# Kernel tuning notes

Hardware: AMD Instinct MI355X
Metric: run time of the kernel (lower is better)

Reference implementation:

```python
import jax, jax.numpy as jnp
import numpy as np

HIGHEST = jax.lax.Precision.HIGHEST
KEY_CHUNK_SIZE = 4096 * 4  # hard-coded in the module's __call__
HEADS = 8
DIM_HEAD = 64


def _query_chunk_size(num_q: int) -> int:
    # replicates the module's static chunk-size selection
    if num_q % 64 == 0:
        return num_q // 64
    if num_q % 16 == 0:
        return num_q // 16
    if num_q % 4 == 0:
        return num_q // 4
    return num_q


def _me_attention(q, k, v, q_chunk: int, k_chunk: int):
    # q, k, v: (S, H, D) where H here is the flattened batch*heads axis
    S, H, D = q.shape
    num_kv = k.shape[0]
    k_chunk = min(k_chunk, num_kv)
    q = q / jnp.sqrt(jnp.asarray(D, q.dtype))
    kc = k.reshape(-1, k_chunk, H, D)          # (nk, kc, H, D)
    vc = v.reshape(-1, k_chunk, H, v.shape[-1])

    def per_qchunk(qch):  # qch: (qc, H, D)
        def summarize(args):
            kch, vch = args
            s = jnp.einsum('qhd,khd->qhk', qch, kch, precision=HIGHEST)
            m = jax.lax.stop_gradient(jnp.max(s, axis=-1, keepdims=True))
            e = jnp.exp(s - m)
            ev = jnp.einsum('khf,qhk->qhf', vch, e, precision=HIGHEST)
            return ev, e.sum(axis=-1), m[..., 0]
        evs, ews, ms = jax.lax.map(summarize, (kc, vc))  # stacked over key chunks
        gm = jnp.max(ms, axis=0)                # (qc, H) global running max
        sc = jnp.exp(ms - gm)                   # (nk, qc, H) rescale factors
        num = (evs * sc[..., None]).sum(axis=0)
        den = (ews * sc).sum(axis=0)
        return num / den[..., None]

    qs = q.reshape(-1, q_chunk, H, D)
    out = jax.lax.map(per_qchunk, qs)           # (nq, qc, H, F)
    return out.reshape(S, H, -1)


def _forward(hidden_states, w_q, w_k, w_v, w_out, b_out):
    B, S, Dm = hidden_states.shape
    H, dh = HEADS, DIM_HEAD
    q = hidden_states @ w_q
    k = hidden_states @ w_k
    v = hidden_states @ w_v

    def to_heads(t):  # (B,S,H*dh) -> (B*H, S, dh)
        return t.reshape(B, S, H, dh).transpose(0, 2, 1, 3).reshape(B * H, S, dh)

    qs, ks, vs = to_heads(q), to_heads(k), to_heads(v)
    # module transposes to (S, B*H, dh) before memory-efficient attention
    qcs = _query_chunk_size(S)
    attn = _me_attention(qs.transpose(1, 0, 2), ks.transpose(1, 0, 2),
                         vs.transpose(1, 0, 2), qcs, KEY_CHUNK_SIZE)
    attn = attn.transpose(1, 0, 2)  # (B*H, S, dh)
    attn = attn.reshape(B, H, S, dh).transpose(0, 2, 1, 3).reshape(B, S, H * dh)
    return attn @ w_out + b_out


def setup_inputs() -> dict:
    key = jax.random.key(0)
    ks = jax.random.split(key, 6)
    B, S, Dm = 2, 8192, 512
    inner = HEADS * DIM_HEAD  # 512
    return {
        'hidden_states': jax.random.normal(ks[0], (B, S, Dm), dtype=jnp.float32),
        'w_q': jax.random.normal(ks[1], (Dm, inner), dtype=jnp.float32) * 0.02,
        'w_k': jax.random.normal(ks[2], (Dm, inner), dtype=jnp.float32) * 0.02,
        'w_v': jax.random.normal(ks[3], (Dm, inner), dtype=jnp.float32) * 0.02,
        'w_out': jax.random.normal(ks[4], (inner, Dm), dtype=jnp.float32) * 0.02,
        'b_out': jnp.zeros((Dm,), dtype=jnp.float32),
    }


def reference(hidden_states, w_q, w_k, w_v, w_out, b_out):
    return _forward(hidden_states, w_q, w_k, w_v, w_out, b_out)
```

## Files before the change

kernel.cpp:

```cpp
#include <hip/hip_runtime.h>
#include <stdint.h>

typedef unsigned short u16;
typedef __attribute__((ext_vector_type(8))) short short8;
typedef __attribute__((ext_vector_type(4))) short short4v;
typedef __attribute__((ext_vector_type(4))) float f32x4;

#define MFMA16(a, b, c) __builtin_amdgcn_mfma_f32_16x16x16bf16_1k(a, b, c, 0, 0, 0)
#define MFMA32(a, b, c) __builtin_amdgcn_mfma_f32_16x16x32_bf16(a, b, c, 0, 0, 0)

#if __has_builtin(__builtin_amdgcn_exp2f)
#define EXP2F(x) __builtin_amdgcn_exp2f(x)
#else
#define EXP2F(x) exp2f(x)
#endif

#define ASYNC16(G, L)                                                            \
    __builtin_amdgcn_global_load_lds((const __attribute__((address_space(1))) void*)(const void*)(G), \
                                     (__attribute__((address_space(3))) void*)(void*)(L), 16, 0, 0)

__device__ __forceinline__ u16 f2bf(float f) {
    union { float f; uint32_t u; } c; c.f = f;
    uint32_t r = (c.u + 0x7fffu + ((c.u >> 16) & 1u)) >> 16;
    return (u16)r;
}

__global__ __launch_bounds__(256) void k_convert_x(const float* __restrict__ X, u16* __restrict__ Xb) {
    int idx = blockIdx.x * 256 + threadIdx.x;
    float4 v = ((const float4*)X)[idx];
    union { u16 s[4]; uint2 v; } u;
    u.s[0] = f2bf(v.x); u.s[1] = f2bf(v.y); u.s[2] = f2bf(v.z); u.s[3] = f2bf(v.w);
    ((uint2*)Xb)[idx] = u.v;
}

__global__ __launch_bounds__(256) void k_convert_w(const float* __restrict__ W0, const float* __restrict__ W1,
                                                   const float* __restrict__ W2, const float* __restrict__ W3,
                                                   u16* __restrict__ Wt) {
    __shared__ u16 T[64][72];
    const float* W = (blockIdx.z == 0) ? W0 : (blockIdx.z == 1) ? W1 : (blockIdx.z == 2) ? W2 : W3;
    int k0 = blockIdx.x * 64, n0 = blockIdx.y * 64;
    int t = threadIdx.x;
    for (int i = 0; i < 4; i++) {
        int id = t + i * 256;
        int row = id >> 4, c4 = (id & 15) * 4;
        float4 v = *(const float4*)(W + (size_t)(k0 + row) * 512 + n0 + c4);
        union { u16 s[4]; uint2 v; } u;
        u.s[0] = f2bf(v.x); u.s[1] = f2bf(v.y); u.s[2] = f2bf(v.z); u.s[3] = f2bf(v.w);
        *(uint2*)&T[row][c4] = u.v;
    }
    __syncthreads();
    u16* O = Wt + (size_t)blockIdx.z * 512 * 512;
    for (int i = 0; i < 2; i++) {
        int id = t + i * 256;
        int row = id >> 3, c8 = (id & 7) * 8;
        union { u16 s[8]; uint4 v; } tmp;
        for (int j = 0; j < 8; j++) tmp.s[j] = T[c8 + j][row];
        *(uint4*)(O + (size_t)(n0 + row) * 512 + k0 + c8) = tmp.v;
    }
}

__global__ __launch_bounds__(256) void k_gemm_qkv(const u16* __restrict__ X, const u16* __restrict__ Wt,
                                                  u16* __restrict__ Q, u16* __restrict__ K, u16* __restrict__ V) {
    __shared__ u16 As[128][40];
    __shared__ u16 Bs[128][40];
    const int t = threadIdx.x;
    const int wave = t >> 6, lane = t & 63, quad = lane >> 4, l16 = lane & 15;
    const int wm = (wave >> 1) * 64, wn = (wave & 1) * 64;
    const int m0 = blockIdx.x * 128, n0 = blockIdx.y * 128;
    const u16* Bt = Wt + (size_t)blockIdx.z * 262144;
    const f32x4 fz = {0.f, 0.f, 0.f, 0.f};
    f32x4 acc[4][4];
    for (int i = 0; i < 4; i++) for (int j = 0; j < 4; j++) acc[i][j] = fz;
    for (int k0 = 0; k0 < 512; k0 += 32) {
        __syncthreads();
        for (int i = 0; i < 2; i++) {
            int id = t + i * 256;
            int row = id >> 2, c8 = (id & 3) * 8;
            *(uint4*)&As[row][c8] = *(const uint4*)(X + (size_t)(m0 + row) * 512 + k0 + c8);
            *(uint4*)&Bs[row][c8] = *(const uint4*)(Bt + (size_t)(n0 + row) * 512 + k0 + c8);
        }
        __syncthreads();
        short8 af[4], bf[4];
        for (int mt = 0; mt < 4; mt++) af[mt] = *(const short8*)&As[wm + mt * 16 + l16][quad * 8];
        for (int nt = 0; nt < 4; nt++) bf[nt] = *(const short8*)&Bs[wn + nt * 16 + l16][quad * 8];
        for (int mt = 0; mt < 4; mt++)
            for (int nt = 0; nt < 4; nt++)
                acc[mt][nt] = MFMA32(af[mt], bf[nt], acc[mt][nt]);
    }
    const float scale = (blockIdx.z == 0) ? 0.18033688011112042f : 1.0f;
    u16* Out = (blockIdx.z == 0) ? Q : (blockIdx.z == 1) ? K : V;
    for (int mt = 0; mt < 4; mt++)
        for (int nt = 0; nt < 4; nt++)
            for (int r = 0; r < 4; r++) {
                int m = m0 + wm + mt * 16 + quad * 4 + r;
                int n = n0 + wn + nt * 16 + l16;
                int b = m >> 13, s = m & 8191, h = n >> 6, d = n & 63;
                Out[((size_t)((b * 8 + h) * 8192 + s)) * 64 + d] = f2bf(acc[mt][nt][r] * scale);
            }
}

__global__ __launch_bounds__(256) void k_transpose_v(const u16* __restrict__ V, u16* __restrict__ Vt) {
    __shared__ u16 T[64][72];
    int s0 = blockIdx.x * 64, bh = blockIdx.y;
    int t = threadIdx.x;
    for (int i = 0; i < 2; i++) {
        int id = t + i * 256, row = id >> 3, c8 = (id & 7) * 8;
        *(uint4*)&T[row][c8] = *(const uint4*)(V + ((size_t)bh * 8192 + s0 + row) * 64 + c8);
    }
    __syncthreads();
    for (int i = 0; i < 2; i++) {
        int id = t + i * 256, row = id >> 3, c8 = (id & 7) * 8;
        union { u16 s[8]; uint4 v; } tmp;
        for (int j = 0; j < 8; j++) tmp.s[j] = T[c8 + j][row];
        *(uint4*)(Vt + ((size_t)bh * 64 + row) * 8192 + s0 + c8) = tmp.v;
    }
}

__global__ __launch_bounds__(256, 4) void k_flash(const u16* __restrict__ Q, const u16* __restrict__ K,
                                                  const u16* __restrict__ Vt, u16* __restrict__ Attn) {
    __shared__ u16 KsAll[2][4096];
    __shared__ u16 VsAll[2][4096];
    const int t = threadIdx.x;
    const int wave = t >> 6, lane = t & 63, quad = lane >> 4, l16 = lane & 15;
    const int l7 = l16 & 7, q1 = quad >> 1, q0 = quad & 1;
    const int qblk = blockIdx.x, bh = blockIdx.y;
    const int b = bh >> 3, h = bh & 7;
    const int q0g = qblk * 128;
    const int mq = wave * 32;
    const u16* Qb = Q + ((size_t)bh * 8192 + q0g) * 64;
    const u16* Kb = K + (size_t)bh * 8192 * 64;
    const u16* Vb = Vt + (size_t)bh * 64 * 8192;

    const int r0 = t >> 3, r1 = (t + 256) >> 3;
    const int x0 = ((t & 7) ^ (r0 & 7)) * 8;
    const int x1 = ((t & 7) ^ (r1 & 7)) * 8;
    const u16* gK0 = Kb + r0 * 64 + x0;
    const u16* gK1 = Kb + r1 * 64 + x1;
    const u16* gV0 = Vb + (size_t)r0 * 8192 + x0;
    const u16* gV1 = Vb + (size_t)r1 * 8192 + x1;
    u16* lK = &KsAll[0][0] + t * 8;
    u16* lV = &VsAll[0][0] + t * 8;

    auto prefetch = [&](int it, int buf) {
        ASYNC16(gK0 + it * 4096, lK + buf * 4096);
        ASYNC16(gK1 + it * 4096, lK + buf * 4096 + 2048);
        ASYNC16(gV0 + it * 64,   lV + buf * 4096);
        ASYNC16(gV1 + it * 64,   lV + buf * 4096 + 2048);
    };

    short8 qf[2][2];
    for (int mt = 0; mt < 2; mt++)
        for (int ks = 0; ks < 2; ks++)
            qf[mt][ks] = *(const short8*)(Qb + (size_t)(mq + mt * 16 + l16) * 64 + ks * 32 + quad * 8);

    const short4v ones = {0x3F80, 0x3F80, 0x3F80, 0x3F80};
    const f32x4 fz = {0.f, 0.f, 0.f, 0.f};
    f32x4 o[2][4], l_i[2];
    for (int mt = 0; mt < 2; mt++) l_i[mt] = fz;
    for (int mt = 0; mt < 2; mt++) for (int nt = 0; nt < 4; nt++) o[mt][nt] = fz;

    prefetch(0, 0);

    auto body = [&](int it, int buf) {
        __syncthreads();
        if (it != 127) prefetch(it + 1, buf ^ 1);
        const u16* KsB = &KsAll[buf][0];
        const u16* VsB = &VsAll[buf][0];

        f32x4 sc[2][4];
        for (int mt = 0; mt < 2; mt++) for (int kt = 0; kt < 4; kt++) sc[mt][kt] = fz;
        for (int ks = 0; ks < 2; ks++)
            for (int kt = 0; kt < 4; kt++) {
                short8 kf = *(const short8*)(KsB + kt * 1024 + l16 * 64 + (((ks * 4 + quad) ^ l7) * 8));
                sc[0][kt] = MFMA32(kf, qf[0][ks], sc[0][kt]);
                sc[1][kt] = MFMA32(kf, qf[1][ks], sc[1][kt]);
            }

        short4v pf[2][4];
        for (int mt = 0; mt < 2; mt++)
            for (int kt = 0; kt < 4; kt++) {
                union { float f; uint32_t u; } e0, e1, e2, e3;
                e0.f = EXP2F(sc[mt][kt][0]);
                e1.f = EXP2F(sc[mt][kt][1]);
                e2.f = EXP2F(sc[mt][kt][2]);
                e3.f = EXP2F(sc[mt][kt][3]);
                union { uint32_t u[2]; short4v s; } pk;
                pk.u[0] = __builtin_amdgcn_perm(e1.u, e0.u, 0x07060302);
                pk.u[1] = __builtin_amdgcn_perm(e3.u, e2.u, 0x07060302);
                pf[mt][kt] = pk.s;
            }

        for (int mt = 0; mt < 2; mt++) {
            f32x4 lacc = fz;
            for (int kt = 0; kt < 4; kt++) lacc = MFMA16(pf[mt][kt], ones, lacc);
            for (int r = 0; r < 4; r++) l_i[mt][r] += lacc[r];
        }

        for (int kt = 0; kt < 4; kt++)
            for (int nt = 0; nt < 4; nt++) {
                short4v vf = *(const short4v*)(VsB + nt * 1024 + l16 * 64 + (((kt * 2 + q1) ^ l7) * 8) + q0 * 4);
                o[0][nt] = MFMA16(pf[0][kt], vf, o[0][nt]);
                o[1][nt] = MFMA16(pf[1][kt], vf, o[1][nt]);
            }
    };

    for (int it2 = 0; it2 < 64; it2++) {
        body(2 * it2, 0);
        body(2 * it2 + 1, 1);
    }

    for (int mt = 0; mt < 2; mt++) {
        f32x4 inv;
        for (int r = 0; r < 4; r++) inv[r] = 1.0f / l_i[mt][r];
        for (int nt = 0; nt < 4; nt++)
            for (int r = 0; r < 4; r++) {
                int sg = q0g + mq + mt * 16 + quad * 4 + r;
                int n = h * 64 + nt * 16 + l16;
                Attn[((size_t)(b * 8192 + sg)) * 512 + n] = f2bf(o[mt][nt][r] * inv[r]);
            }
    }
}

__global__ __launch_bounds__(256) void k_gemm_out(const u16* __restrict__ A, const u16* __restrict__ Wot,
                                                  const float* __restrict__ bias, float* __restrict__ Out) {
    __shared__ u16 As[128][40];
    __shared__ u16 Bs[128][40];
    const int t = threadIdx.x;
    const int wave = t >> 6, lane = t & 63, quad = lane >> 4, l16 = lane & 15;
    const int wm = (wave >> 1) * 64, wn = (wave & 1) * 64;
    const int m0 = blockIdx.x * 128, n0 = blockIdx.y * 128;
    const f32x4 fz = {0.f, 0.f, 0.f, 0.f};
    f32x4 acc[4][4];
    for (int i = 0; i < 4; i++) for (int j = 0; j < 4; j++) acc[i][j] = fz;
    for (int k0 = 0; k0 < 512; k0 += 32) {
        __syncthreads();
        for (int i = 0; i < 2; i++) {
            int id = t + i * 256;
            int row = id >> 2, c8 = (id & 3) * 8;
            *(uint4*)&As[row][c8] = *(const uint4*)(A + (size_t)(m0 + row) * 512 + k0 + c8);
            *(uint4*)&Bs[row][c8] = *(const uint4*)(Wot + (size_t)(n0 + row) * 512 + k0 + c8);
        }
        __syncthreads();
        short8 af[4], bf[4];
        for (int mt = 0; mt < 4; mt++) af[mt] = *(const short8*)&As[wm + mt * 16 + l16][quad * 8];
        for (int nt = 0; nt < 4; nt++) bf[nt] = *(const short8*)&Bs[wn + nt * 16 + l16][quad * 8];
        for (int mt = 0; mt < 4; mt++)
            for (int nt = 0; nt < 4; nt++)
                acc[mt][nt] = MFMA32(af[mt], bf[nt], acc[mt][nt]);
    }
    float bv[4];
    for (int nt = 0; nt < 4; nt++) bv[nt] = bias[n0 + wn + nt * 16 + l16];
    for (int mt = 0; mt < 4; mt++)
        for (int nt = 0; nt < 4; nt++)
            for (int r = 0; r < 4; r++) {
                int m = m0 + wm + mt * 16 + quad * 4 + r;
                int n = n0 + wn + nt * 16 + l16;
                Out[(size_t)m * 512 + n] = acc[mt][nt][r] + bv[nt];
            }
}

extern "C" void kernel_launch(void* const* d_in, const int* in_sizes, int n_in,
                              void* d_out, int out_size, void* d_ws, size_t ws_size,
                              hipStream_t stream) {
    const float* X   = (const float*)d_in[0];
    const float* w_q = (const float*)d_in[1];
    const float* w_k = (const float*)d_in[2];
    const float* w_v = (const float*)d_in[3];
    const float* w_o = (const float*)d_in[4];
    const float* b_o = (const float*)d_in[5];
    float* Out = (float*)d_out;

    char* ws = (char*)d_ws;
    u16* Xb   = (u16*)(ws);
    u16* Wt   = (u16*)(ws + 16777216);
    u16* Qd   = (u16*)(ws + 18874368);
    u16* Kd   = (u16*)(ws + 35651584);
    u16* Vd   = (u16*)(ws + 52428800);
    u16* Vtd  = (u16*)(ws + 69206016);
    u16* Attn = Xb;

    hipLaunchKernelGGL(k_convert_x, dim3(8192), dim3(256), 0, stream, X, Xb);
    hipLaunchKernelGGL(k_convert_w, dim3(8, 8, 4), dim3(256), 0, stream, w_q, w_k, w_v, w_o, Wt);
    hipLaunchKernelGGL(k_gemm_qkv, dim3(128, 4, 3), dim3(256), 0, stream, Xb, Wt, Qd, Kd, Vd);
    hipLaunchKernelGGL(k_transpose_v, dim3(128, 16), dim3(256), 0, stream, Vd, Vtd);
    hipLaunchKernelGGL(k_flash, dim3(64, 16), dim3(256), 0, stream, Qd, Kd, Vtd, Attn);
    hipLaunchKernelGGL(k_gemm_out, dim3(128, 4), dim3(256), 0, stream, Attn, Wt + 3 * 262144, b_o, Out);
}
```

Baseline: 464.2 us.

## Widen flash block to 8 waves sharing K/V tiles; compute row sums on VALU

The attention kernel now launches 512-thread blocks covering 256 queries instead of 256-thread blocks covering 128. Eight waves share each staged K/V tile, which halves global-to-LDS traffic per query, and each thread issues one async load per tensor per step instead of two. The softmax denominator is no longer computed with extra MFMAs against a ones vector. Each lane accumulates scalar exp sums instead, and the per-query totals are combined with cross-lane shuffles in the epilogue. In exchange, larger blocks with launch bounds (512,4) may raise register pressure or lower scheduling flexibility, and the VALU adds take the place of the matrix-core work.

```diff
diff --git a/kernel.cpp b/kernel.cpp
--- a/kernel.cpp
+++ b/kernel.cpp
@@ -116,36 +116,31 @@
     }
 }
 
-__global__ __launch_bounds__(256, 4) void k_flash(const u16* __restrict__ Q, const u16* __restrict__ K,
+__global__ __launch_bounds__(512, 4) void k_flash(const u16* __restrict__ Q, const u16* __restrict__ K,
                                                   const u16* __restrict__ Vt, u16* __restrict__ Attn) {
     __shared__ u16 KsAll[2][4096];
     __shared__ u16 VsAll[2][4096];
     const int t = threadIdx.x;
     const int wave = t >> 6, lane = t & 63, quad = lane >> 4, l16 = lane & 15;
-    const int l7 = l16 & 7, q1 = quad >> 1, q0 = quad & 1;
+    const int l7 = l16 & 7, q1 = quad >> 1, qlo = quad & 1;
     const int qblk = blockIdx.x, bh = blockIdx.y;
     const int b = bh >> 3, h = bh & 7;
-    const int q0g = qblk * 128;
+    const int q0g = qblk * 256;
     const int mq = wave * 32;
     const u16* Qb = Q + ((size_t)bh * 8192 + q0g) * 64;
     const u16* Kb = K + (size_t)bh * 8192 * 64;
     const u16* Vb = Vt + (size_t)bh * 64 * 8192;
 
-    const int r0 = t >> 3, r1 = (t + 256) >> 3;
+    const int r0 = t >> 3;
     const int x0 = ((t & 7) ^ (r0 & 7)) * 8;
-    const int x1 = ((t & 7) ^ (r1 & 7)) * 8;
     const u16* gK0 = Kb + r0 * 64 + x0;
-    const u16* gK1 = Kb + r1 * 64 + x1;
     const u16* gV0 = Vb + (size_t)r0 * 8192 + x0;
-    const u16* gV1 = Vb + (size_t)r1 * 8192 + x1;
     u16* lK = &KsAll[0][0] + t * 8;
     u16* lV = &VsAll[0][0] + t * 8;
 
     auto prefetch = [&](int it, int buf) {
         ASYNC16(gK0 + it * 4096, lK + buf * 4096);
-        ASYNC16(gK1 + it * 4096, lK + buf * 4096 + 2048);
         ASYNC16(gV0 + it * 64,   lV + buf * 4096);
-        ASYNC16(gV1 + it * 64,   lV + buf * 4096 + 2048);
     };
 
     short8 qf[2][2];
@@ -153,10 +148,9 @@
         for (int ks = 0; ks < 2; ks++)
             qf[mt][ks] = *(const short8*)(Qb + (size_t)(mq + mt * 16 + l16) * 64 + ks * 32 + quad * 8);
 
-    const short4v ones = {0x3F80, 0x3F80, 0x3F80, 0x3F80};
     const f32x4 fz = {0.f, 0.f, 0.f, 0.f};
-    f32x4 o[2][4], l_i[2];
-    for (int mt = 0; mt < 2; mt++) l_i[mt] = fz;
+    f32x4 o[2][4];
+    float l_i[2] = {0.f, 0.f};
     for (int mt = 0; mt < 2; mt++) for (int nt = 0; nt < 4; nt++) o[mt][nt] = fz;
 
     prefetch(0, 0);
@@ -168,13 +162,14 @@
         const u16* VsB = &VsAll[buf][0];
 
         f32x4 sc[2][4];
-        for (int mt = 0; mt < 2; mt++) for (int kt = 0; kt < 4; kt++) sc[mt][kt] = fz;
-        for (int ks = 0; ks < 2; ks++)
-            for (int kt = 0; kt < 4; kt++) {
-                short8 kf = *(const short8*)(KsB + kt * 1024 + l16 * 64 + (((ks * 4 + quad) ^ l7) * 8));
-                sc[0][kt] = MFMA32(kf, qf[0][ks], sc[0][kt]);
-                sc[1][kt] = MFMA32(kf, qf[1][ks], sc[1][kt]);
-            }
+        for (int kt = 0; kt < 4; kt++) {
+            short8 kf0 = *(const short8*)(KsB + kt * 1024 + l16 * 64 + (((0 * 4 + quad) ^ l7) * 8));
+            short8 kf1 = *(const short8*)(KsB + kt * 1024 + l16 * 64 + (((1 * 4 + quad) ^ l7) * 8));
+            sc[0][kt] = MFMA32(kf0, qf[0][0], fz);
+            sc[1][kt] = MFMA32(kf0, qf[1][0], fz);
+            sc[0][kt] = MFMA32(kf1, qf[0][1], sc[0][kt]);
+            sc[1][kt] = MFMA32(kf1, qf[1][1], sc[1][kt]);
+        }
 
         short4v pf[2][4];
         for (int mt = 0; mt < 2; mt++)
@@ -184,21 +179,16 @@
                 e1.f = EXP2F(sc[mt][kt][1]);
                 e2.f = EXP2F(sc[mt][kt][2]);
                 e3.f = EXP2F(sc[mt][kt][3]);
+                l_i[mt] += (e0.f + e1.f) + (e2.f + e3.f);
                 union { uint32_t u[2]; short4v s; } pk;
                 pk.u[0] = __builtin_amdgcn_perm(e1.u, e0.u, 0x07060302);
                 pk.u[1] = __builtin_amdgcn_perm(e3.u, e2.u, 0x07060302);
                 pf[mt][kt] = pk.s;
             }
 
-        for (int mt = 0; mt < 2; mt++) {
-            f32x4 lacc = fz;
-            for (int kt = 0; kt < 4; kt++) lacc = MFMA16(pf[mt][kt], ones, lacc);
-            for (int r = 0; r < 4; r++) l_i[mt][r] += lacc[r];
-        }
-
         for (int kt = 0; kt < 4; kt++)
             for (int nt = 0; nt < 4; nt++) {
-                short4v vf = *(const short4v*)(VsB + nt * 1024 + l16 * 64 + (((kt * 2 + q1) ^ l7) * 8) + q0 * 4);
+                short4v vf = *(const short4v*)(VsB + nt * 1024 + l16 * 64 + (((kt * 2 + q1) ^ l7) * 8) + qlo * 4);
                 o[0][nt] = MFMA16(pf[0][kt], vf, o[0][nt]);
                 o[1][nt] = MFMA16(pf[1][kt], vf, o[1][nt]);
             }
@@ -210,13 +200,17 @@
     }
 
     for (int mt = 0; mt < 2; mt++) {
-        f32x4 inv;
-        for (int r = 0; r < 4; r++) inv[r] = 1.0f / l_i[mt][r];
+        float l = l_i[mt];
+        l += __shfl_xor(l, 16);
+        l += __shfl_xor(l, 32);
+        float inv = 1.0f / l;
+        float invC[4];
+        for (int r = 0; r < 4; r++) invC[r] = __shfl(inv, quad * 4 + r);
         for (int nt = 0; nt < 4; nt++)
             for (int r = 0; r < 4; r++) {
                 int sg = q0g + mq + mt * 16 + quad * 4 + r;
                 int n = h * 64 + nt * 16 + l16;
-                Attn[((size_t)(b * 8192 + sg)) * 512 + n] = f2bf(o[mt][nt][r] * inv[r]);
+                Attn[((size_t)(b * 8192 + sg)) * 512 + n] = f2bf(o[mt][nt][r] * invC[r]);
             }
     }
 }
@@ -283,6 +277,6 @@
     hipLaunchKernelGGL(k_convert_w, dim3(8, 8, 4), dim3(256), 0, stream, w_q, w_k, w_v, w_o, Wt);
     hipLaunchKernelGGL(k_gemm_qkv, dim3(128, 4, 3), dim3(256), 0, stream, Xb, Wt, Qd, Kd, Vd);
     hipLaunchKernelGGL(k_transpose_v, dim3(128, 16), dim3(256), 0, stream, Vd, Vtd);
-    hipLaunchKernelGGL(k_flash, dim3(64, 16), dim3(256), 0, stream, Qd, Kd, Vtd, Attn);
+    hipLaunchKernelGGL(k_flash, dim3(32, 16), dim3(512), 0, stream, Qd, Kd, Vtd, Attn);
     hipLaunchKernelGGL(k_gemm_out, dim3(128, 4), dim3(256), 0, stream, Attn, Wt + 3 * 262144, b_o, Out);
 }
```

New measurement: 433.3 us. 1.07x faster.
